# Kernel tuning notes

Measured on AMD Instinct MI355X. Metric: run time of the kernel, lower is better.

Reference implementation:

```python
import jax, jax.numpy as jnp
import numpy as np

B, T, N, C, H, K = 32, 12, 512, 2, 64, 3
P = C + H  # 66, GCN input feature dim


def _xavier(key, fan_in, fan_out):
    std = (2.0 / (fan_in + fan_out)) ** 0.5
    return jax.random.normal(key, (fan_in, fan_out), dtype=jnp.float32) * std


def setup_inputs() -> dict:
    key = jax.random.key(0)
    k1, k2, k3, k4 = jax.random.split(key, 4)
    # scale adjacency so K-hop aggregation stays O(1) in magnitude
    G = jax.random.normal(k1, (K, N, N), dtype=jnp.float32) * (1.0 / np.sqrt(N))
    x_seq = jax.random.normal(k2, (B, T, N, C), dtype=jnp.float32)
    init_h = jnp.zeros((B, N, H), dtype=jnp.float32)
    W_gate = _xavier(k3, K * P, 2 * H)
    b_gate = jnp.zeros((2 * H,), dtype=jnp.float32)
    W_update = _xavier(k4, K * P, H)
    b_update = jnp.zeros((H,), dtype=jnp.float32)
    return {"G": G, "x_seq": x_seq, "init_h": init_h,
            "W_gate": W_gate, "b_gate": b_gate,
            "W_update": W_update, "b_update": b_update}


def _gcn(G, x, W, b):
    # x: [B, N, P]; G: [K, N, N] -> support_cat: [B, N, K*P] (k-major, matching torch cat order)
    Bq, Nq, Pq = x.shape
    sup = jnp.einsum('kij,bjp->bikp', G, x).reshape(Bq, Nq, -1)
    return sup @ W + b


def _cell(G, x, h, Wg, bg, Wu, bu):
    combined = jnp.concatenate([x, h], axis=-1)             # [B,N,C+H]
    zr = jax.nn.sigmoid(_gcn(G, combined, Wg, bg))           # [B,N,2H]
    z, r = zr[..., :H], zr[..., H:]
    candidate = jnp.concatenate([x, r * h], axis=-1)
    hc = jnp.tanh(_gcn(G, candidate, Wu, bu))
    return (1.0 - z) * h + z * hc


def reference(G, x_seq, init_h, W_gate, b_gate, W_update, b_update):
    # scan over time (sequential GRU state dependency)
    xs = jnp.swapaxes(x_seq, 0, 1)  # [T,B,N,C]

    def step(h, x_t):
        h2 = _cell(G, x_t, h, W_gate, b_gate, W_update, b_update)
        return h2, None

    h_last, _ = jax.lax.scan(step, init_h, xs)
    return h_last  # [B,N,H] — last hidden state of the (single) layer
```

## Files before the change

### kernel.cpp

```cpp
#include <hip/hip_runtime.h>
#include <hip/hip_bf16.h>
#include <cmath>

#define NN 512
#define BB 32
#define HH 64
#define TT 12
#define KS 3

#define OFF_GHI   0
#define OFF_GPK   786432
#define OFF_XTH   1572864
#define OFF_XTL   1769472
#define OFF_SX    1966080
#define OFF_HHI   3145728
#define OFF_HLO   3670016
#define OFF_RHHI  4194304
#define OFF_Z     4718592
#define OFF_WHGH  6291456
#define OFF_WHGL  6304256
#define OFF_WHUH  6317056
#define OFF_WHUL  6323456
#define OFF_WXG   6329856
#define OFF_WXU   6330624

typedef __attribute__((ext_vector_type(8))) short v8s;
typedef __attribute__((ext_vector_type(4))) float f32x4;
typedef __attribute__((ext_vector_type(4))) unsigned short u16x4;

__device__ __forceinline__ unsigned short f2bf(float f) {
  union { __hip_bfloat16 h; unsigned short u; } x;
  x.h = __float2bfloat16(f);
  return x.u;
}
__device__ __forceinline__ float bf2f(unsigned short u) {
  union { unsigned short u; __hip_bfloat16 h; } x;
  x.u = u;
  return __bfloat162float(x.h);
}

__device__ __forceinline__ int swz64(int j, int key) {
  return (j & ~63) | ((((j >> 3) & 7) ^ key) << 3) | (j & 7);
}

__device__ __forceinline__ void gl_lds16(const unsigned short* g, short* l) {
  __builtin_amdgcn_global_load_lds(
      (const __attribute__((address_space(1))) void*)g,
      (__attribute__((address_space(3))) void*)l, 16, 0, 0);
}

__device__ __forceinline__ float fast_tanh(float x) {
  float e = __expf(2.f * x);
  return 1.f - 2.f / (e + 1.f);
}

__global__ __launch_bounds__(256) void prep_all(
    const float* __restrict__ G, const float* __restrict__ x_seq,
    const float* __restrict__ init_h, const float* __restrict__ Wg,
    const float* __restrict__ Wu,
    unsigned short* __restrict__ Ghi, unsigned short* __restrict__ Gpk,
    unsigned short* __restrict__ Xh, unsigned short* __restrict__ Xl,
    unsigned short* __restrict__ Hhi, unsigned short* __restrict__ Hlo,
    unsigned short* __restrict__ Whgh, unsigned short* __restrict__ Whgl,
    unsigned short* __restrict__ Whuh, unsigned short* __restrict__ Whul,
    float* __restrict__ Wxg, float* __restrict__ Wxu) {
  int idx = blockIdx.x * 256 + threadIdx.x;
  if (idx < 786432) {
    int j = idx & 511;
    int i = (idx >> 9) & 511;
    Ghi[(size_t)(idx >> 9) * 512 + swz64(j, i & 7)] = f2bf(G[idx]);
  } else if (idx < 884736) {
    int t = idx - 786432;
    int L = t & 63;
    int frag = t >> 6;
    int m = frag % 3;
    int kf = (frag / 3) & 1;
    int j0 = (frag / 6) & 7;
    int i0w = frag / 48;
    int w = i0w & 3, i0 = i0w >> 2;
    int R = w * 48 + m * 16 + (L & 15);
    int ksec = R >> 6;
    int i = i0 * 64 + (R & 63);
    int jb = j0 * 64 + kf * 32 + (L >> 4) * 8;
    unsigned short* dst = Gpk + (size_t)frag * 512 + L * 8;
#pragma unroll
    for (int e = 0; e < 8; ++e) dst[e] = f2bf(G[((size_t)ksec * NN + i) * NN + jb + e]);
  } else if (idx < 1277952) {
    int t2 = idx - 884736;
    int j = t2 & 511;
    int col = t2 >> 9;
    int t = col >> 6;
    int b = (col & 63) >> 1;
    int c = col & 1;
    float v = x_seq[((size_t)(b * TT + t) * NN + j) * 2 + c];
    unsigned short hi = f2bf(v);
    size_t pos = (size_t)col * 512 + swz64(j, col & 7);
    Xh[pos] = hi;
    Xl[pos] = f2bf(v - bf2f(hi));
  } else if (idx < 2326528) {
    int t2 = idx - 1277952;
    int i = t2 & 511;
    int col = t2 >> 9;
    int b = col >> 6;
    int p = col & 63;
    float h = init_h[((size_t)b * NN + i) * HH + p];
    unsigned short hi = f2bf(h);
    size_t pos = (size_t)col * 512 + swz64(i, col & 7);
    Hhi[pos] = hi;
    Hlo[pos] = f2bf(h - bf2f(hi));
  } else if (idx < 2364544) {
    int j2 = idx - 2326528;
    if (j2 < 24576) {
      int o = j2 & 127, kq = j2 >> 7;
      int k = kq >> 6, q = kq & 63;
      float v = Wg[(size_t)(k * 66 + 2 + q) * 128 + o];
      unsigned short hi = f2bf(v);
      Whgh[o * 200 + kq] = hi;
      Whgl[o * 200 + kq] = f2bf(v - bf2f(hi));
    } else if (j2 < 36864) {
      int j = j2 - 24576;
      int o = j & 63, kq = j >> 6;
      int k = kq >> 6, q = kq & 63;
      float v = Wu[(size_t)(k * 66 + 2 + q) * 64 + o];
      unsigned short hi = f2bf(v);
      Whuh[o * 200 + kq] = hi;
      Whul[o * 200 + kq] = f2bf(v - bf2f(hi));
    } else if (j2 < 37632) {
      int j = j2 - 36864;
      int o = j & 127, kc = j >> 7;
      Wxg[kc * 128 + o] = Wg[(size_t)((kc >> 1) * 66 + (kc & 1)) * 128 + o];
    } else {
      int j = j2 - 37632;
      int o = j & 63, kc = j >> 6;
      Wxu[kc * 64 + o] = Wu[(size_t)((kc >> 1) * 66 + (kc & 1)) * 64 + o];
    }
  }
}

__global__ __launch_bounds__(256) void gemm_sx(const unsigned short* __restrict__ Ghi,
                                               const unsigned short* __restrict__ Xh,
                                               const unsigned short* __restrict__ Xl,
                                               float* __restrict__ Sx2) {
  __shared__ __align__(16) short sA[64 * 64];
  __shared__ __align__(16) short sB[64 * 64];
  int tid = threadIdx.x;
  int L = tid & 63, w = tid >> 6;
  int wm = (w >> 1) * 32, wn = (w & 1) * 32;
  int i0 = blockIdx.y * 64;
  int c0 = blockIdx.x * 64;
  f32x4 acc[2][2];
#pragma unroll
  for (int m = 0; m < 2; ++m)
#pragma unroll
    for (int n = 0; n < 2; ++n) acc[m][n] = (f32x4)(0.f);

  for (int j0 = 0; j0 < 1024; j0 += 64) {
    const unsigned short* Bsel = (j0 < 512) ? Xh : Xl;
    int jb = j0 & 511;
    __syncthreads();
#pragma unroll
    for (int u = 0; u < 2; ++u) {
      int r = w * 16 + u * 8;
      gl_lds16(Ghi + (size_t)(i0 + r + (L >> 3)) * 512 + jb + (L & 7) * 8, sA + r * 64);
      gl_lds16(Bsel + (size_t)(c0 + r + (L >> 3)) * 512 + jb + (L & 7) * 8, sB + r * 64);
    }
    __syncthreads();
#pragma unroll
    for (int kf = 0; kf < 2; ++kf) {
      int kog = kf * 4 + (L >> 4);
      v8s af[2], bf[2];
#pragma unroll
      for (int m = 0; m < 2; ++m) {
        int row = wm + m * 16 + (L & 15);
        af[m] = *(const v8s*)(sA + row * 64 + ((kog ^ (row & 7)) << 3));
      }
#pragma unroll
      for (int n = 0; n < 2; ++n) {
        int row = wn + n * 16 + (L & 15);
        bf[n] = *(const v8s*)(sB + row * 64 + ((kog ^ (row & 7)) << 3));
      }
#pragma unroll
      for (int m = 0; m < 2; ++m)
#pragma unroll
        for (int n = 0; n < 2; ++n)
          acc[m][n] = __builtin_amdgcn_mfma_f32_16x16x32_bf16(af[m], bf[n], acc[m][n], 0, 0, 0);
    }
  }
#pragma unroll
  for (int m = 0; m < 2; ++m)
#pragma unroll
    for (int r = 0; r < 4; ++r)
#pragma unroll
      for (int n = 0; n < 2; ++n)
        Sx2[(size_t)(i0 + wm + m * 16 + (L >> 4) * 4 + r) * 768 + c0 + wn + n * 16 + (L & 15)] =
            acc[m][n][r];
}

template <int GATE>
__global__ __launch_bounds__(512, 2) void fused_step(
    const unsigned short* __restrict__ Gpk,
    const unsigned short* __restrict__ Bhi,
    const float* __restrict__ Sx2,
    const unsigned short* __restrict__ Whi,
    const unsigned short* __restrict__ Wlo,
    const float* __restrict__ Wx,
    const float* __restrict__ bias,
    const unsigned short* __restrict__ Hr_hi,
    const unsigned short* __restrict__ Hr_lo,
    unsigned short* __restrict__ Ohi,
    unsigned short* __restrict__ Olo,
    float* __restrict__ Z,
    float* __restrict__ out, int t) {
  constexpr int O = GATE ? 128 : 64;
  constexpr int NF = GATE ? 4 : 2;
  __shared__ __align__(16) char smem[67584];
  short* sBh = (short*)smem;
  short* sS  = (short*)smem;
  float* sSx = (float*)(smem + 65536);

  int tid = threadIdx.x;
  int L = tid & 63, w = tid >> 6;
  int wm = w & 3, wn = w >> 2;
  int bid = blockIdx.x;
  int xcd = bid & 7, local = bid >> 3;
  int b = xcd * 4 + (local >> 3);
  int i0t = local & 7;
  int i0 = i0t * 64;
  int bcol = b * 64;
  const unsigned short* Ap = Gpk + (size_t)(i0t * 4 + wm) * 48 * 512;

#pragma unroll
  for (int u = 0; u < 8; ++u) {
    int col = w * 8 + u;
    gl_lds16(Bhi + (size_t)(bcol + col) * 512 + L * 8, sBh + col * 512);
  }
  for (int e = tid; e < 384; e += 512) {
    int il = e / 6, kc = e % 6;
    sSx[e] = Sx2[(size_t)((kc >> 1) * 512 + i0 + il) * 768 + t * 64 + b * 2 + (kc & 1)];
  }
  __syncthreads();

  f32x4 acc[3][2];
#pragma unroll
  for (int m = 0; m < 3; ++m)
#pragma unroll
    for (int n = 0; n < 2; ++n) acc[m][n] = (f32x4)(0.f);
#pragma unroll
  for (int it = 0; it < 8; ++it) {
    v8s ah[2][3];
#pragma unroll
    for (int kf = 0; kf < 2; ++kf)
#pragma unroll
      for (int m = 0; m < 3; ++m)
        ah[kf][m] = *(const v8s*)(Ap + (size_t)((it * 2 + kf) * 3 + m) * 512 + L * 8);
#pragma unroll
    for (int kf = 0; kf < 2; ++kf) {
      int jj = it * 64 + kf * 32 + (L >> 4) * 8;
      v8s bh[2];
#pragma unroll
      for (int n = 0; n < 2; ++n) {
        int col = wn * 32 + n * 16 + (L & 15);
        int off = col * 512 + ((jj & ~63) | (((((jj >> 3) & 7) ^ (col & 7))) << 3));
        bh[n] = *(const v8s*)(sBh + off);
      }
#pragma unroll
      for (int m = 0; m < 3; ++m)
#pragma unroll
        for (int n = 0; n < 2; ++n)
          acc[m][n] = __builtin_amdgcn_mfma_f32_16x16x32_bf16(ah[kf][m], bh[n], acc[m][n], 0, 0, 0);
    }
  }
  __syncthreads();

#pragma unroll
  for (int m = 0; m < 3; ++m)
#pragma unroll
    for (int n = 0; n < 2; ++n)
#pragma unroll
      for (int r = 0; r < 4; ++r) {
        int R = wm * 48 + m * 16 + (L >> 4) * 4 + r;
        int il = R & 63, kk = R >> 6;
        int p = wn * 32 + n * 16 + (L & 15);
        float v = acc[m][n][r];
        unsigned short hi = f2bf(v);
        sS[il * 408 + kk * 64 + p] = (short)hi;
        sS[il * 408 + 200 + kk * 64 + p] = (short)f2bf(v - bf2f(hi));
      }
  __syncthreads();

  int me = w & 3, oh = w >> 2;
  f32x4 acc2[NF];
#pragma unroll
  for (int n = 0; n < NF; ++n) acc2[n] = (f32x4)(0.f);
#pragma unroll
  for (int s = 0; s < 3; ++s) {
    const unsigned short* Wsrc = (s < 2) ? Whi : Wlo;
    int abase = (s == 1) ? 200 : 0;
#pragma unroll
    for (int f = 0; f < 6; ++f) {
      int k0 = f * 32 + (L >> 4) * 8;
      v8s af2 = *(const v8s*)(sS + (me * 16 + (L & 15)) * 408 + abase + k0);
#pragma unroll
      for (int n = 0; n < NF; ++n) {
        v8s bf2 = *(const v8s*)(Wsrc + (size_t)(oh * (O / 2) + n * 16 + (L & 15)) * 200 + k0);
        acc2[n] = __builtin_amdgcn_mfma_f32_16x16x32_bf16(af2, bf2, acc2[n], 0, 0, 0);
      }
    }
  }

#pragma unroll
  for (int n = 0; n < NF; ++n) {
    int o = oh * (O / 2) + n * 16 + (L & 15);
    int il0 = me * 16 + (L >> 4) * 4;
    float vals[4];
#pragma unroll
    for (int r = 0; r < 4; ++r) {
      float v = acc2[n][r] + bias[o];
#pragma unroll
      for (int kc = 0; kc < 6; ++kc) v += sSx[(il0 + r) * 6 + kc] * Wx[kc * O + o];
      vals[r] = v;
    }
    if (GATE) {
      float sg[4];
#pragma unroll
      for (int r = 0; r < 4; ++r) sg[r] = 1.f / (1.f + __expf(-vals[r]));
      if (oh == 0) {
#pragma unroll
        for (int r = 0; r < 4; ++r)
          Z[((size_t)b * 512 + i0 + il0 + r) * 64 + o] = sg[r];
      } else {
        int col = bcol + (o - 64);
        size_t cb = (size_t)col * 512 + i0 + (((il0 >> 3) ^ (col & 7)) << 3) + (il0 & 7);
        u16x4 h4 = *(const u16x4*)(Hr_hi + cb);
        u16x4 l4 = *(const u16x4*)(Hr_lo + cb);
        u16x4 oh4;
#pragma unroll
        for (int r = 0; r < 4; ++r) {
          float h = bf2f(h4[r]) + bf2f(l4[r]);
          oh4[r] = f2bf(sg[r] * h);
        }
        *(u16x4*)(Ohi + cb) = oh4;
      }
    } else {
      int col = bcol + o;
      size_t cb = (size_t)col * 512 + i0 + (((il0 >> 3) ^ (col & 7)) << 3) + (il0 & 7);
      u16x4 h4 = *(const u16x4*)(Hr_hi + cb);
      u16x4 l4 = *(const u16x4*)(Hr_lo + cb);
      u16x4 oh4, ol4;
#pragma unroll
      for (int r = 0; r < 4; ++r) {
        float hc = fast_tanh(vals[r]);
        float z = Z[((size_t)b * 512 + i0 + il0 + r) * 64 + o];
        float h = bf2f(h4[r]) + bf2f(l4[r]);
        float hn = (1.f - z) * h + z * hc;
        unsigned short hi = f2bf(hn);
        oh4[r] = hi;
        ol4[r] = f2bf(hn - bf2f(hi));
        if (t == TT - 1) out[((size_t)b * 512 + i0 + il0 + r) * 64 + o] = hn;
      }
      *(u16x4*)(Ohi + cb) = oh4;
      *(u16x4*)(Olo + cb) = ol4;
    }
  }
}

extern "C" void kernel_launch(void* const* d_in, const int* in_sizes, int n_in,
                              void* d_out, int out_size, void* d_ws, size_t ws_size,
                              hipStream_t stream) {
  const float* G      = (const float*)d_in[0];
  const float* x_seq  = (const float*)d_in[1];
  const float* init_h = (const float*)d_in[2];
  const float* Wg     = (const float*)d_in[3];
  const float* bg     = (const float*)d_in[4];
  const float* Wu     = (const float*)d_in[5];
  const float* bu     = (const float*)d_in[6];
  float* out = (float*)d_out;
  float* ws = (float*)d_ws;

  unsigned short* GHI  = (unsigned short*)(ws + OFF_GHI);
  unsigned short* GPK  = (unsigned short*)(ws + OFF_GPK);
  unsigned short* Xh   = (unsigned short*)(ws + OFF_XTH);
  unsigned short* Xl   = (unsigned short*)(ws + OFF_XTL);
  float* Sx2           = ws + OFF_SX;
  unsigned short* Hhi  = (unsigned short*)(ws + OFF_HHI);
  unsigned short* Hlo  = (unsigned short*)(ws + OFF_HLO);
  unsigned short* RHhi = (unsigned short*)(ws + OFF_RHHI);
  float* Z             = ws + OFF_Z;
  unsigned short* Whgh = (unsigned short*)(ws + OFF_WHGH);
  unsigned short* Whgl = (unsigned short*)(ws + OFF_WHGL);
  unsigned short* Whuh = (unsigned short*)(ws + OFF_WHUH);
  unsigned short* Whul = (unsigned short*)(ws + OFF_WHUL);
  float* Wxg           = ws + OFF_WXG;
  float* Wxu           = ws + OFF_WXU;

  prep_all<<<9237, 256, 0, stream>>>(G, x_seq, init_h, Wg, Wu, GHI, GPK, Xh, Xl,
                                     Hhi, Hlo, Whgh, Whgl, Whuh, Whul, Wxg, Wxu);
  gemm_sx<<<dim3(12, 24), 256, 0, stream>>>(GHI, Xh, Xl, Sx2);

  for (int t = 0; t < TT; ++t) {
    fused_step<1><<<256, 512, 0, stream>>>(GPK, Hhi, Sx2, Whgh, Whgl, Wxg, bg,
                                           Hhi, Hlo, RHhi, RHhi, Z, out, t);
    fused_step<0><<<256, 512, 0, stream>>>(GPK, RHhi, Sx2, Whuh, Whul, Wxu, bu,
                                           Hhi, Hlo, Hhi, Hlo, Z, out, t);
  }
}
```

Before: 358.1 us.

## Drop low-bf16 split for x, store gate z as bf16, remap block-to-XCD

Removes the hi/lo bf16 split of x_seq, so the precomputed G·x GEMM runs over half the reduction length. The gate z is stored as bf16 instead of fp32, which halves that intermediate's write and read traffic. The block index mapping is changed so each XCD group covers 8 batches and half of the row tiles, which changes how G tiles and H columns are shared in cache. Both precision reductions lower accuracy in the recurrence and could accumulate error across 12 timesteps.

```diff
diff --git a/kernel.cpp b/kernel.cpp
--- a/kernel.cpp
+++ b/kernel.cpp
@@ -11,7 +11,6 @@
 #define OFF_GHI   0
 #define OFF_GPK   786432
 #define OFF_XTH   1572864
-#define OFF_XTL   1769472
 #define OFF_SX    1966080
 #define OFF_HHI   3145728
 #define OFF_HLO   3670016
@@ -59,7 +58,7 @@
     const float* __restrict__ init_h, const float* __restrict__ Wg,
     const float* __restrict__ Wu,
     unsigned short* __restrict__ Ghi, unsigned short* __restrict__ Gpk,
-    unsigned short* __restrict__ Xh, unsigned short* __restrict__ Xl,
+    unsigned short* __restrict__ Xh,
     unsigned short* __restrict__ Hhi, unsigned short* __restrict__ Hlo,
     unsigned short* __restrict__ Whgh, unsigned short* __restrict__ Whgl,
     unsigned short* __restrict__ Whuh, unsigned short* __restrict__ Whul,
@@ -93,10 +92,7 @@
     int b = (col & 63) >> 1;
     int c = col & 1;
     float v = x_seq[((size_t)(b * TT + t) * NN + j) * 2 + c];
-    unsigned short hi = f2bf(v);
-    size_t pos = (size_t)col * 512 + swz64(j, col & 7);
-    Xh[pos] = hi;
-    Xl[pos] = f2bf(v - bf2f(hi));
+    Xh[(size_t)col * 512 + swz64(j, col & 7)] = f2bf(v);
   } else if (idx < 2326528) {
     int t2 = idx - 1277952;
     int i = t2 & 511;
@@ -139,7 +135,6 @@
 
 __global__ __launch_bounds__(256) void gemm_sx(const unsigned short* __restrict__ Ghi,
                                                const unsigned short* __restrict__ Xh,
-                                               const unsigned short* __restrict__ Xl,
                                                float* __restrict__ Sx2) {
   __shared__ __align__(16) short sA[64 * 64];
   __shared__ __align__(16) short sB[64 * 64];
@@ -154,15 +149,13 @@
 #pragma unroll
     for (int n = 0; n < 2; ++n) acc[m][n] = (f32x4)(0.f);
 
-  for (int j0 = 0; j0 < 1024; j0 += 64) {
-    const unsigned short* Bsel = (j0 < 512) ? Xh : Xl;
-    int jb = j0 & 511;
+  for (int j0 = 0; j0 < 512; j0 += 64) {
     __syncthreads();
 #pragma unroll
     for (int u = 0; u < 2; ++u) {
       int r = w * 16 + u * 8;
-      gl_lds16(Ghi + (size_t)(i0 + r + (L >> 3)) * 512 + jb + (L & 7) * 8, sA + r * 64);
-      gl_lds16(Bsel + (size_t)(c0 + r + (L >> 3)) * 512 + jb + (L & 7) * 8, sB + r * 64);
+      gl_lds16(Ghi + (size_t)(i0 + r + (L >> 3)) * 512 + j0 + (L & 7) * 8, sA + r * 64);
+      gl_lds16(Xh + (size_t)(c0 + r + (L >> 3)) * 512 + j0 + (L & 7) * 8, sB + r * 64);
     }
     __syncthreads();
 #pragma unroll
@@ -209,7 +202,7 @@
     const unsigned short* __restrict__ Hr_lo,
     unsigned short* __restrict__ Ohi,
     unsigned short* __restrict__ Olo,
-    float* __restrict__ Z,
+    unsigned short* __restrict__ Z,
     float* __restrict__ out, int t) {
   constexpr int O = GATE ? 128 : 64;
   constexpr int NF = GATE ? 4 : 2;
@@ -222,9 +215,10 @@
   int L = tid & 63, w = tid >> 6;
   int wm = w & 3, wn = w >> 2;
   int bid = blockIdx.x;
-  int xcd = bid & 7, local = bid >> 3;
-  int b = xcd * 4 + (local >> 3);
-  int i0t = local & 7;
+  int c = bid & 7, local = bid >> 3;
+  int p = c >> 1, hc = c & 1;
+  int b = p * 8 + (local >> 2);
+  int i0t = hc * 4 + (local & 3);
   int i0 = i0t * 64;
   int bcol = b * 64;
   const unsigned short* Ap = Gpk + (size_t)(i0t * 4 + wm) * 48 * 512;
@@ -280,11 +274,11 @@
       for (int r = 0; r < 4; ++r) {
         int R = wm * 48 + m * 16 + (L >> 4) * 4 + r;
         int il = R & 63, kk = R >> 6;
-        int p = wn * 32 + n * 16 + (L & 15);
+        int pp = wn * 32 + n * 16 + (L & 15);
         float v = acc[m][n][r];
         unsigned short hi = f2bf(v);
-        sS[il * 408 + kk * 64 + p] = (short)hi;
-        sS[il * 408 + 200 + kk * 64 + p] = (short)f2bf(v - bf2f(hi));
+        sS[il * 408 + kk * 64 + pp] = (short)hi;
+        sS[il * 408 + 200 + kk * 64 + pp] = (short)f2bf(v - bf2f(hi));
       }
   __syncthreads();
 
@@ -327,7 +321,7 @@
       if (oh == 0) {
 #pragma unroll
         for (int r = 0; r < 4; ++r)
-          Z[((size_t)b * 512 + i0 + il0 + r) * 64 + o] = sg[r];
+          Z[((size_t)b * 512 + i0 + il0 + r) * 64 + o] = f2bf(sg[r]);
       } else {
         int col = bcol + (o - 64);
         size_t cb = (size_t)col * 512 + i0 + (((il0 >> 3) ^ (col & 7)) << 3) + (il0 & 7);
@@ -349,10 +343,10 @@
       u16x4 oh4, ol4;
 #pragma unroll
       for (int r = 0; r < 4; ++r) {
-        float hc = fast_tanh(vals[r]);
-        float z = Z[((size_t)b * 512 + i0 + il0 + r) * 64 + o];
+        float hc2 = fast_tanh(vals[r]);
+        float z = bf2f(Z[((size_t)b * 512 + i0 + il0 + r) * 64 + o]);
         float h = bf2f(h4[r]) + bf2f(l4[r]);
-        float hn = (1.f - z) * h + z * hc;
+        float hn = (1.f - z) * h + z * hc2;
         unsigned short hi = f2bf(hn);
         oh4[r] = hi;
         ol4[r] = f2bf(hn - bf2f(hi));
@@ -380,12 +374,11 @@
   unsigned short* GHI  = (unsigned short*)(ws + OFF_GHI);
   unsigned short* GPK  = (unsigned short*)(ws + OFF_GPK);
   unsigned short* Xh   = (unsigned short*)(ws + OFF_XTH);
-  unsigned short* Xl   = (unsigned short*)(ws + OFF_XTL);
   float* Sx2           = ws + OFF_SX;
   unsigned short* Hhi  = (unsigned short*)(ws + OFF_HHI);
   unsigned short* Hlo  = (unsigned short*)(ws + OFF_HLO);
   unsigned short* RHhi = (unsigned short*)(ws + OFF_RHHI);
-  float* Z             = ws + OFF_Z;
+  unsigned short* Z    = (unsigned short*)(ws + OFF_Z);
   unsigned short* Whgh = (unsigned short*)(ws + OFF_WHGH);
   unsigned short* Whgl = (unsigned short*)(ws + OFF_WHGL);
   unsigned short* Whuh = (unsigned short*)(ws + OFF_WHUH);
@@ -393,9 +386,9 @@
   float* Wxg           = ws + OFF_WXG;
   float* Wxu           = ws + OFF_WXU;
 
-  prep_all<<<9237, 256, 0, stream>>>(G, x_seq, init_h, Wg, Wu, GHI, GPK, Xh, Xl,
+  prep_all<<<9237, 256, 0, stream>>>(G, x_seq, init_h, Wg, Wu, GHI, GPK, Xh,
                                      Hhi, Hlo, Whgh, Whgl, Whuh, Whul, Wxg, Wxu);
-  gemm_sx<<<dim3(12, 24), 256, 0, stream>>>(GHI, Xh, Xl, Sx2);
+  gemm_sx<<<dim3(12, 24), 256, 0, stream>>>(GHI, Xh, Sx2);
 
   for (int t = 0; t < TT; ++t) {
     fused_step<1><<<256, 512, 0, stream>>>(GPK, Hhi, Sx2, Whgh, Whgl, Wxg, bg,
```

Result: no change. 361.4 us (+0.9%).
